# Kernel optimization log

Measured on AMD Instinct MI355X. Metric: run time of the kernel, lower is better.

## Reference

```python
import jax, jax.numpy as jnp
import numpy as np

MARGIN = 0.2


def setup_inputs() -> dict:
    key = jax.random.key(0)
    ks = jax.random.split(key, 6)
    B, E = 8192, 1024
    return {
        "A_is_t": jax.random.normal(ks[0], (B, E), dtype=jnp.float32),
        "A_em_t": jax.random.normal(ks[1], (B, E), dtype=jnp.float32),
        "m": jax.random.normal(ks[2], (B, E), dtype=jnp.float32),
        "tr_m": jax.random.normal(ks[3], (B, E), dtype=jnp.float32),
        "W": jax.random.normal(ks[4], (E, E), dtype=jnp.float32) * (1.0 / np.sqrt(E)),
        "b": jax.random.normal(ks[5], (E,), dtype=jnp.float32) * 0.01,
    }


def reference(A_is_t, A_em_t, m, tr_m, W, b):
    # Linear layer: w(A) = A @ W.T + b  (torch nn.Linear convention)
    wA_is = A_is_t @ W.T + b  # [B, E]
    wA_em = A_em_t @ W.T + b  # [B, E]
    # Original builds full [B,B] score matrices but only uses the diagonal;
    # diagonal entries are exactly rowwise dots, computed directly here.
    d_is = jnp.einsum("be,be->b", m, wA_is)
    d_em = jnp.einsum("be,be->b", m, wA_em)
    d_is_trm = jnp.einsum("be,be->b", tr_m, wA_is)
    d_em_trm = jnp.einsum("be,be->b", tr_m, wA_em)
    diag_is_all = 0.4 * d_is + 0.6 * d_is_trm  # [B]
    diag_em_all = 0.6 * d_em_trm + 0.4 * d_em  # [B]
    cost_s = jnp.maximum(MARGIN + diag_is_all - diag_em_all, 0.0)  # hinge
    return cost_s.reshape(-1, 1).sum(axis=0)  # [1], matches cost_s.sum(0)
```

## Files before the change

### kernel.cpp

```cpp
#include <hip/hip_runtime.h>
#include <hip/hip_bf16.h>
#include <hip/hip_fp8.h>

#define B_ROWS 8192
#define E_DIM  1024
#define MARGIN 0.2f
#define BK 64
#define NSTEPS (E_DIM / BK)
#define WSCALE 16.0f

typedef float f32x4 __attribute__((ext_vector_type(4)));

__device__ __forceinline__ void gload_lds16(const void* g, void* l) {
    __builtin_amdgcn_global_load_lds(
        (__attribute__((address_space(1))) void*)(g),
        (__attribute__((address_space(3))) void*)(l),
        16, 0, 0);
}

#define GATE4() do { asm volatile("s_waitcnt vmcnt(4)" ::: "memory"); \
                     __builtin_amdgcn_sched_barrier(0); } while (0)
#define GATE0() do { asm volatile("s_waitcnt vmcnt(0)" ::: "memory"); \
                     __builtin_amdgcn_sched_barrier(0); } while (0)
#define RBAR()  do { __builtin_amdgcn_s_barrier(); \
                     __builtin_amdgcn_sched_barrier(0); } while (0)
#define LGKM0() do { asm volatile("s_waitcnt lgkmcnt(0)" ::: "memory"); \
                     __builtin_amdgcn_sched_barrier(0); } while (0)

__device__ __forceinline__ unsigned char to_fp8(float x) {
    return __hip_fp8_e4m3(x).__x;
}

__global__ __launch_bounds__(256)
void prep_combo(const float* __restrict__ m, const float* __restrict__ trm,
                unsigned char* __restrict__ c8p,
                const float* __restrict__ W, unsigned char* __restrict__ wtp,
                float* __restrict__ delta) {
    const int tid = threadIdx.x;
    const int mi  = tid >> 6;
    const int l   = tid & 63;
    const int lr  = l & 15;
    const int hi  = l >> 4;
    if (blockIdx.x < 4096) {
        const int unit  = blockIdx.x;
        const int panel = unit >> 5;
        const int kt    = unit & 31;
        const size_t g  = (size_t)(panel * 64 + mi * 16 + lr) * E_DIM + kt * 32 + hi * 8;
        float4 m0 = *(const float4*)(m + g);
        float4 m1 = *(const float4*)(m + g + 4);
        float4 t0 = *(const float4*)(trm + g);
        float4 t1 = *(const float4*)(trm + g + 4);
        union { unsigned char b[8]; unsigned long long u; } r;
        r.b[0] = to_fp8(0.4f*m0.x + 0.6f*t0.x);
        r.b[1] = to_fp8(0.4f*m0.y + 0.6f*t0.y);
        r.b[2] = to_fp8(0.4f*m0.z + 0.6f*t0.z);
        r.b[3] = to_fp8(0.4f*m0.w + 0.6f*t0.w);
        r.b[4] = to_fp8(0.4f*m1.x + 0.6f*t1.x);
        r.b[5] = to_fp8(0.4f*m1.y + 0.6f*t1.y);
        r.b[6] = to_fp8(0.4f*m1.z + 0.6f*t1.z);
        r.b[7] = to_fp8(0.4f*m1.w + 0.6f*t1.w);
        *(unsigned long long*)(c8p + (size_t)unit * 2048 + mi * 512 + l * 8) = r.u;
    } else if (blockIdx.x < 4608) {
        const int unit = blockIdx.x - 4096;
        const int np   = unit >> 5;
        const int kt   = unit & 31;
        const int n    = np * 64 + mi * 16 + lr;
        const int k0   = kt * 32 + hi * 8;
        union { unsigned char b[8]; unsigned long long u; } r;
#pragma unroll
        for (int j = 0; j < 8; ++j)
            r.b[j] = to_fp8(W[(size_t)(k0 + j) * E_DIM + n] * WSCALE);
        *(unsigned long long*)(wtp + (size_t)unit * 2048 + mi * 512 + l * 8) = r.u;
    } else {
        delta[(blockIdx.x - 4608) * 256 + threadIdx.x] = 0.f;
    }
}

__global__ __launch_bounds__(256)
void gemm_dot(const unsigned char* __restrict__ c8p, const unsigned char* __restrict__ wtp,
              const float* __restrict__ Ais, const float* __restrict__ Aem,
              float* __restrict__ delta) {
    __shared__ char smem[49152];

    const int tid  = threadIdx.x;
    const int lane = tid & 63;
    const int lr   = lane & 15;
    const int hi   = lane >> 4;
    const int wave = tid >> 6;
    const int wr   = wave >> 1, wc = wave & 1;

    const int bid = blockIdx.x;
    const int xcd = bid & 7;
    const int q   = bid >> 3;
    const int rb  = (xcd * 8 + (q >> 3)) * 128;
    const int cb  = (q & 7) * 128;
    const int ap0 = rb >> 6;
    const int bp0 = cb >> 6;

    auto stage = [&](int slot, int t) {
#pragma unroll
        for (int j = 0; j < 2; ++j) {
            const int off = j * 4096 + tid * 16;
            const int u   = off >> 11;
            const int w   = off & 2047;
            const size_t gA = ((size_t)(ap0 + (u >> 1)) * 32 + (2 * t + (u & 1))) * 2048 + w;
            const size_t gB = ((size_t)(bp0 + (u >> 1)) * 32 + (2 * t + (u & 1))) * 2048 + w;
            gload_lds16(c8p + gA, smem + slot * 16384 + off);
            gload_lds16(wtp + gB, smem + slot * 16384 + 8192 + off);
        }
    };

    f32x4 acc[4][4] = {};

    stage(0, 0);
    stage(1, 1);

    int s0 = 0, s1 = 1, s2 = 2;
    for (int t = 0; t < NSTEPS; ++t) {
        if (t + 1 < NSTEPS) GATE4(); else GATE0();
        RBAR();

        const char* Ab = smem + s0 * 16384;
        const char* Bb = Ab + 8192;
        long a[4][2], b[4][2];
#pragma unroll
        for (int kk = 0; kk < 2; ++kk) {
            const int au = (wr * 2 + kk) * 2048 + lane * 8;
            const int bu = (wc * 2 + kk) * 2048 + lane * 8;
#pragma unroll
            for (int mi = 0; mi < 4; ++mi) a[mi][kk] = *(const long*)(Ab + au + mi * 512);
#pragma unroll
            for (int ni = 0; ni < 4; ++ni) b[ni][kk] = *(const long*)(Bb + bu + ni * 512);
        }
        LGKM0();

        if (t + 2 < NSTEPS) stage(s2, t + 2);

        __builtin_amdgcn_s_setprio(1);
#pragma unroll
        for (int kk = 0; kk < 2; ++kk)
#pragma unroll
            for (int mi = 0; mi < 4; ++mi)
#pragma unroll
                for (int ni = 0; ni < 4; ++ni)
                    acc[mi][ni] = __builtin_amdgcn_mfma_f32_16x16x32_fp8_fp8(
                        a[mi][kk], b[ni][kk], acc[mi][ni], 0, 0, 0);
        __builtin_amdgcn_s_setprio(0);

        int tmp = s0; s0 = s1; s1 = s2; s2 = tmp;
    }

    const int colbase = cb + wc * 64 + lr;
    const int rowbase = rb + wr * 64 + hi * 4;
#pragma unroll
    for (int mi = 0; mi < 4; ++mi) {
#pragma unroll
        for (int jj = 0; jj < 4; ++jj) {
            const int r = rowbase + mi * 16 + jj;
            float v = 0.f;
#pragma unroll
            for (int ni = 0; ni < 4; ++ni) {
                const size_t idx = (size_t)r * E_DIM + colbase + ni * 16;
                v += acc[mi][ni][jj] * (Ais[idx] - Aem[idx]);
            }
            v += __shfl_xor(v, 1);
            v += __shfl_xor(v, 2);
            v += __shfl_xor(v, 4);
            v += __shfl_xor(v, 8);
            if (lr == 0) atomicAdd(&delta[r], v * (1.0f / WSCALE));
        }
    }
}

__global__ void hinge_sum(const float* __restrict__ delta, float* __restrict__ out) {
    float s = 0.f;
    for (int i = threadIdx.x; i < B_ROWS; i += 256)
        s += fmaxf(MARGIN + delta[i], 0.f);
#pragma unroll
    for (int off = 32; off > 0; off >>= 1) s += __shfl_down(s, off);
    __shared__ float wsum[4];
    int lane = threadIdx.x & 63, w = threadIdx.x >> 6;
    if (lane == 0) wsum[w] = s;
    __syncthreads();
    if (threadIdx.x == 0) out[0] = wsum[0] + wsum[1] + wsum[2] + wsum[3];
}

extern "C" void kernel_launch(void* const* d_in, const int* in_sizes, int n_in,
                              void* d_out, int out_size, void* d_ws, size_t ws_size,
                              hipStream_t stream) {
    const float* A_is = (const float*)d_in[0];
    const float* A_em = (const float*)d_in[1];
    const float* m    = (const float*)d_in[2];
    const float* tr_m = (const float*)d_in[3];
    const float* W    = (const float*)d_in[4];
    float* out = (float*)d_out;

    char* ws = (char*)d_ws;
    unsigned char* c8p = (unsigned char*)ws;
    unsigned char* wtp = (unsigned char*)(ws + (size_t)8 * 1024 * 1024);
    float*         delta = (float*)(ws + (size_t)9 * 1024 * 1024);

    prep_combo<<<4640, 256, 0, stream>>>(m, tr_m, c8p, W, wtp, delta);
    gemm_dot<<<512, 256, 0, stream>>>(c8p, wtp, A_is, A_em, delta);
    hinge_sum<<<1, 256, 0, stream>>>(delta, out);
}
```

Before: 51.27 us.

## Prefetch epilogue A_is/A_em loads during GEMM main loop via inline asm

Moves the epilogue's global reads of A_is and A_em into the K-loop. Each step issues 8 raw global_load_dword instructions for four elements, double-buffered in registers, and accumulates the differences into a 64-entry register array. The loop is fully unrolled and the vmcnt waits are adjusted to cover the extra outstanding loads. This hides the epilogue's scattered load latency behind the MFMA work, but adds register pressure and depends on hand-counted vmcnt ordering being correct.

```diff
diff --git a/kernel.cpp b/kernel.cpp
--- a/kernel.cpp
+++ b/kernel.cpp
@@ -18,14 +18,14 @@
         16, 0, 0);
 }
 
-#define GATE4() do { asm volatile("s_waitcnt vmcnt(4)" ::: "memory"); \
-                     __builtin_amdgcn_sched_barrier(0); } while (0)
-#define GATE0() do { asm volatile("s_waitcnt vmcnt(0)" ::: "memory"); \
+#define GATE(N) do { asm volatile("s_waitcnt vmcnt(" #N ")" ::: "memory"); \
                      __builtin_amdgcn_sched_barrier(0); } while (0)
 #define RBAR()  do { __builtin_amdgcn_s_barrier(); \
                      __builtin_amdgcn_sched_barrier(0); } while (0)
 #define LGKM0() do { asm volatile("s_waitcnt lgkmcnt(0)" ::: "memory"); \
                      __builtin_amdgcn_sched_barrier(0); } while (0)
+#define LOADF(dst, addr) \
+    asm volatile("global_load_dword %0, %1, off" : "=v"(dst) : "v"(addr))
 
 __device__ __forceinline__ unsigned char to_fp8(float x) {
     return __hip_fp8_e4m3(x).__x;
@@ -97,6 +97,11 @@
     const int ap0 = rb >> 6;
     const int bp0 = cb >> 6;
 
+    const int rowbase = rb + wr * 64 + hi * 4;
+    const int colbase = cb + wc * 64 + lr;
+    const unsigned long long isb = (unsigned long long)(uintptr_t)Ais;
+    const unsigned long long emb = (unsigned long long)(uintptr_t)Aem;
+
     auto stage = [&](int slot, int t) {
 #pragma unroll
         for (int j = 0; j < 2; ++j) {
@@ -111,16 +116,26 @@
     };
 
     f32x4 acc[4][4] = {};
+    float diff[64];
+    float tis[8], tem[8];
 
     stage(0, 0);
     stage(1, 1);
 
-    int s0 = 0, s1 = 1, s2 = 2;
+#pragma unroll
     for (int t = 0; t < NSTEPS; ++t) {
-        if (t + 1 < NSTEPS) GATE4(); else GATE0();
+        if (t == 0)                 GATE(4);
+        else if (t == NSTEPS - 1)   GATE(8);
+        else                        GATE(12);
         RBAR();
 
-        const char* Ab = smem + s0 * 16384;
+        if (t >= 2) {
+#pragma unroll
+            for (int r = 0; r < 4; ++r)
+                diff[(t - 2) * 4 + r] = tis[(t & 1) * 4 + r] - tem[(t & 1) * 4 + r];
+        }
+
+        const char* Ab = smem + (t % 3) * 16384;
         const char* Bb = Ab + 8192;
         long a[4][2], b[4][2];
 #pragma unroll
@@ -134,7 +149,20 @@
         }
         LGKM0();
 
-        if (t + 2 < NSTEPS) stage(s2, t + 2);
+        if (t + 2 < NSTEPS) stage((t + 2) % 3, t + 2);
+
+        {
+#pragma unroll
+            for (int r = 0; r < 4; ++r) {
+                const int qq = t * 4 + r;
+                const int mi = qq >> 4, jj = (qq >> 2) & 3, ni = qq & 3;
+                const unsigned long long off =
+                    ((unsigned long long)(rowbase + mi * 16 + jj) * E_DIM
+                     + colbase + ni * 16) * 4ull;
+                LOADF(tis[(t & 1) * 4 + r], isb + off);
+                LOADF(tem[(t & 1) * 4 + r], emb + off);
+            }
+        }
 
         __builtin_amdgcn_s_setprio(1);
 #pragma unroll
@@ -146,12 +174,15 @@
                     acc[mi][ni] = __builtin_amdgcn_mfma_f32_16x16x32_fp8_fp8(
                         a[mi][kk], b[ni][kk], acc[mi][ni], 0, 0, 0);
         __builtin_amdgcn_s_setprio(0);
-
-        int tmp = s0; s0 = s1; s1 = s2; s2 = tmp;
     }
 
-    const int colbase = cb + wc * 64 + lr;
-    const int rowbase = rb + wr * 64 + hi * 4;
+    GATE(0);
+#pragma unroll
+    for (int b2 = NSTEPS - 2; b2 < NSTEPS; ++b2)
+#pragma unroll
+        for (int r = 0; r < 4; ++r)
+            diff[b2 * 4 + r] = tis[(b2 & 1) * 4 + r] - tem[(b2 & 1) * 4 + r];
+
 #pragma unroll
     for (int mi = 0; mi < 4; ++mi) {
 #pragma unroll
@@ -159,10 +190,8 @@
             const int r = rowbase + mi * 16 + jj;
             float v = 0.f;
 #pragma unroll
-            for (int ni = 0; ni < 4; ++ni) {
-                const size_t idx = (size_t)r * E_DIM + colbase + ni * 16;
-                v += acc[mi][ni][jj] * (Ais[idx] - Aem[idx]);
-            }
+            for (int ni = 0; ni < 4; ++ni)
+                v += acc[mi][ni][jj] * diff[mi * 16 + jj * 4 + ni];
             v += __shfl_xor(v, 1);
             v += __shfl_xor(v, 2);
             v += __shfl_xor(v, 4);
```

Result: slower. 54.09 us (+5.5%).
